# Optimization experiments

Measured on AMD Instinct MI355X. Metric: run time of the kernel, lower is better.

Reference implementation:

```python
import jax, jax.numpy as jnp
import numpy as np

B, T, C, H = 2, 2048, 1024, 16
D = C // H  # 64 per-head dim


def setup_inputs() -> dict:
    key = jax.random.key(0)
    ks = jax.random.split(key, 9)
    s = 1.0 / np.sqrt(C)
    return {
        "query_src": jax.random.normal(ks[0], (B, T, C), jnp.float32),
        "key_src": jax.random.normal(ks[1], (B, T, C), jnp.float32),
        "value_src": jax.random.normal(ks[2], (B, T, C), jnp.float32),
        "Wq": jax.random.normal(ks[3], (C, C), jnp.float32) * s,
        "Wk": jax.random.normal(ks[4], (C, C), jnp.float32) * s,
        "Wv": jax.random.normal(ks[5], (C, C), jnp.float32) * s,
        "Wo": jax.random.normal(ks[6], (C, C), jnp.float32) * s,
        "bo": jax.random.normal(ks[7], (C,), jnp.float32) * s,
    }


def reference(query_src, key_src, value_src, Wq, Wk, Wv, Wo, bo):
    # Linear layers: y = x @ W.T (torch nn.Linear convention)
    q = jnp.einsum('btc,dc->btd', query_src, Wq).reshape(B, T, H, D).transpose(0, 2, 1, 3)
    k = jnp.einsum('btc,dc->btd', key_src, Wk).reshape(B, T, H, D).transpose(0, 2, 1, 3)
    v = jnp.einsum('btc,dc->btd', value_src, Wv).reshape(B, T, H, D).transpose(0, 2, 1, 3)
    # scores: [B, H, T, T]
    scores = jnp.einsum('bhqd,bhkd->bhqk', q, k)
    # FAITHFUL quirk: original divides by d**(-0.5) => multiplies by sqrt(D)
    scores = scores * jnp.sqrt(jnp.asarray(D, scores.dtype))
    # FAITHFUL quirk: softmax over dim=1 == the HEAD axis
    attn = jax.nn.softmax(scores, axis=1)
    # dropout is identity in eval mode
    out = jnp.einsum('bhqk,bhkd->bhqd', attn, v)  # [B,H,T,D]
    out = out.transpose(0, 2, 1, 3).reshape(B, T, C)
    return jnp.einsum('btc,dc->btd', out, Wo) + bo
```

## Files before the change

### kernel.cpp

```cpp
#include <hip/hip_runtime.h>
#include <cmath>

namespace {

constexpr int B_ = 2;
constexpr int T_ = 2048;
constexpr int C_ = 1024;
constexpr int H_ = 16;
constexpr int D_ = 64;

typedef _Float16 half8 __attribute__((ext_vector_type(8)));
typedef _Float16 half4 __attribute__((ext_vector_type(4)));
typedef float f32x4 __attribute__((ext_vector_type(4)));

__device__ inline f32x4 vmax4(f32x4 a, f32x4 b) {
  f32x4 r;
  r[0] = fmaxf(a[0], b[0]); r[1] = fmaxf(a[1], b[1]);
  r[2] = fmaxf(a[2], b[2]); r[3] = fmaxf(a[3], b[3]);
  return r;
}

__device__ __forceinline__ void gload16(const _Float16* g, _Float16* l) {
  __builtin_amdgcn_global_load_lds(
      (const __attribute__((address_space(1))) unsigned int*)g,
      (__attribute__((address_space(3))) unsigned int*)l, 16, 0, 0);
}

__device__ __forceinline__ void lds_barrier() {
  asm volatile("s_waitcnt lgkmcnt(0)" ::: "memory");
  __builtin_amdgcn_s_barrier();
}

__global__ __launch_bounds__(256)
void cast7(const float* __restrict__ xq, const float* __restrict__ xk,
           const float* __restrict__ xv, const float* __restrict__ wq,
           const float* __restrict__ wk, const float* __restrict__ wv,
           const float* __restrict__ wo,
           _Float16* __restrict__ dxq, _Float16* __restrict__ dxk,
           _Float16* __restrict__ dxv, _Float16* __restrict__ dwq,
           _Float16* __restrict__ dwk, _Float16* __restrict__ dwv,
           _Float16* __restrict__ dwo) {
  constexpr size_t NX = (size_t)4 << 20;
  constexpr size_t NW = (size_t)1 << 20;
  size_t g = ((size_t)blockIdx.x * 256 + threadIdx.x) * 8;
  const float* s; _Float16* d; size_t off;
  if      (g <     NX)          { s = xq; d = dxq; off = g; }
  else if (g < 2 * NX)          { s = xk; d = dxk; off = g - NX; }
  else if (g < 3 * NX)          { s = xv; d = dxv; off = g - 2 * NX; }
  else if (g < 3 * NX + NW)     { s = wq; d = dwq; off = g - 3 * NX; }
  else if (g < 3 * NX + 2 * NW) { s = wk; d = dwk; off = g - 3 * NX - NW; }
  else if (g < 3 * NX + 3 * NW) { s = wv; d = dwv; off = g - 3 * NX - 2 * NW; }
  else                          { s = wo; d = dwo; off = g - 3 * NX - 3 * NW; }
  const float4 a = *(const float4*)(s + off);
  const float4 b = *(const float4*)(s + off + 4);
  half8 h;
  h[0] = (_Float16)a.x; h[1] = (_Float16)a.y; h[2] = (_Float16)a.z; h[3] = (_Float16)a.w;
  h[4] = (_Float16)b.x; h[5] = (_Float16)b.y; h[6] = (_Float16)b.z; h[7] = (_Float16)b.w;
  *(half8*)(d + off) = h;
}

__global__ __launch_bounds__(256, 3)
void gemm_f16nt(const _Float16* __restrict__ A0, const _Float16* __restrict__ A1,
                const _Float16* __restrict__ A2,
                const _Float16* __restrict__ W0, const _Float16* __restrict__ W1,
                const _Float16* __restrict__ W2,
                _Float16* __restrict__ Y0, _Float16* __restrict__ Y1,
                _Float16* __restrict__ Y2,
                float* __restrict__ Yf, const float* __restrict__ bias,
                int K, int N, int mode, float qsc) {
  __shared__ _Float16 sA[128 * 32];
  __shared__ _Float16 sW[128 * 32];

  const int tid  = threadIdx.x;
  const int lane = tid & 63;
  const int w    = tid >> 6;
  const int l15  = lane & 15;
  const int quad = lane >> 4;
  const int z    = blockIdx.z;
  const _Float16* A = (z == 0) ? A0 : (z == 1) ? A1 : A2;
  const _Float16* W = (z == 0) ? W0 : (z == 1) ? W1 : W2;
  _Float16*       Y = (z == 0) ? Y0 : (z == 1) ? Y1 : Y2;

  const int m0 = blockIdx.y * 128;
  const int n0 = blockIdx.x * 128;

  const int Rb  = lane >> 2;
  const int pch = lane & 3;
  const int lch = pch ^ ((Rb >> 1) & 3);
  const int swr = (l15 >> 1) & 3;

  f32x4 acc[4][4];
#pragma unroll
  for (int mt = 0; mt < 4; ++mt)
#pragma unroll
    for (int nt = 0; nt < 4; ++nt)
      acc[mt][nt] = (f32x4){0.f, 0.f, 0.f, 0.f};

  const int wm = (w >> 1) * 64;
  const int wn = (w & 1) * 64;

  for (int k0 = 0; k0 < K; k0 += 32) {
    __syncthreads();
#pragma unroll
    for (int j = 0; j < 2; ++j) {
      const int seg = w * 32 + j * 16;
      gload16(A + (size_t)(m0 + seg + Rb) * K + k0 + lch * 8, &sA[seg * 32]);
      gload16(W + (size_t)(n0 + seg + Rb) * K + k0 + lch * 8, &sW[seg * 32]);
    }
    __syncthreads();

    half8 af[4], wf[4];
#pragma unroll
    for (int mt = 0; mt < 4; ++mt) {
      const int R = wm + mt * 16 + l15;
      af[mt] = *(const half8*)&sA[R * 32 + (quad ^ swr) * 8];
    }
#pragma unroll
    for (int nt = 0; nt < 4; ++nt) {
      const int R = wn + nt * 16 + l15;
      wf[nt] = *(const half8*)&sW[R * 32 + (quad ^ swr) * 8];
    }
#pragma unroll
    for (int mt = 0; mt < 4; ++mt)
#pragma unroll
      for (int nt = 0; nt < 4; ++nt)
        acc[mt][nt] = __builtin_amdgcn_mfma_f32_16x16x32_f16(wf[nt], af[mt], acc[mt][nt], 0, 0, 0);
  }

  const float ysc = (mode == 0 && z == 0) ? qsc : 1.f;
#pragma unroll
  for (int mt = 0; mt < 4; ++mt)
#pragma unroll
    for (int nt = 0; nt < 4; ++nt) {
      const int m = m0 + wm + mt * 16 + l15;
      const int n = n0 + wn + nt * 16 + quad * 4;
      if (mode == 2) {
        float4 v;
        v.x = acc[mt][nt][0] + bias[n + 0];
        v.y = acc[mt][nt][1] + bias[n + 1];
        v.z = acc[mt][nt][2] + bias[n + 2];
        v.w = acc[mt][nt][3] + bias[n + 3];
        *(float4*)(Yf + (size_t)m * N + n) = v;
      } else {
        half4 hv;
#pragma unroll
        for (int r = 0; r < 4; ++r) hv[r] = (_Float16)(acc[mt][nt][r] * ysc);
        *(half4*)(Y + (size_t)m * N + n) = hv;
      }
    }
}

__global__ __launch_bounds__(256)
void transpose_v(const _Float16* __restrict__ Vh, _Float16* __restrict__ Vt) {
  constexpr int PAD = 1028;
  __shared__ _Float16 tile[16][PAD];
  const int b  = blockIdx.x >> 7;
  const int kt = blockIdx.x & 127;
  const int tid = threadIdx.x;

#pragma unroll
  for (int j = 0; j < 8; ++j) {
    const int ch = tid + 256 * j;
    const int t  = ch >> 7;
    const int c8 = ch & 127;
    *(half8*)&tile[t][c8 * 8] =
        *(const half8*)(Vh + ((size_t)b * T_ + kt * 16 + t) * C_ + c8 * 8);
  }
  __syncthreads();

#pragma unroll
  for (int j = 0; j < 8; ++j) {
    const int cc = tid + 256 * j;
    const int h  = cc >> 7;
    const int d  = (cc >> 1) & 63;
    const int th = (cc & 1) * 8;
    const int c  = h * 64 + d;
    half4 va, vb4;
#pragma unroll
    for (int i = 0; i < 4; ++i) va[i]  = tile[th + i][c];
#pragma unroll
    for (int i = 0; i < 4; ++i) vb4[i] = tile[th + 4 + i][c];
    const size_t tb = (((size_t)b * H_ + h) * 128 + kt) * 1024;
    const int nb = ((d >> 5) & 1) * 512 + ((th >> 2) * 16 + (d & 15)) * 8 +
                   ((d >> 4) & 1) * 4;
    *(half4*)(Vt + tb + nb) = va;
    *(half4*)(Vt + tb + nb + 128) = vb4;
  }
}

__global__ __launch_bounds__(1024, 4)
void attn_mfma(const _Float16* __restrict__ Qhp, const _Float16* __restrict__ Khp,
               const _Float16* __restrict__ Vtp, _Float16* __restrict__ OP,
               int nsplit) {
  __shared__ _Float16 sK[16 * 1024];
  __shared__ _Float16 sV[2][16][1024];
  __shared__ f32x4 redm[4][4][64];
  __shared__ f32x4 reds[4][4][64];

  const int tid  = threadIdx.x;
  const int lane = tid & 63;
  const int w    = tid >> 6;
  const int qt   = w >> 2;
  const int wg   = w & 3;
  const int l15  = lane & 15;
  const int quad = lane >> 4;
  const int cell = quad * 16 + l15;

  const int nbq   = B_ * (T_ / 64);
  const int split = blockIdx.x / nbq;
  const int bq    = blockIdx.x % nbq;
  const int b  = bq >> 5;
  const int q0 = (bq & 31) << 6;

  const size_t qrow = ((size_t)b * T_ + q0 + qt * 16 + l15) * C_;
  half8 qh[4][2];
#pragma unroll
  for (int hl = 0; hl < 4; ++hl)
#pragma unroll
    for (int kk = 0; kk < 2; ++kk)
      qh[hl][kk] = *(const half8*)(Qhp + qrow + (wg * 4 + hl) * 64 + kk * 32 + quad * 8);

  f32x4 oacc[4][4];
#pragma unroll
  for (int hl = 0; hl < 4; ++hl)
#pragma unroll
    for (int mt = 0; mt < 4; ++mt)
      oacc[hl][mt] = (f32x4){0.f, 0.f, 0.f, 0.f};

  const int kpb  = T_ / nsplit;
  const int k_lo = split * kpb;
  const int jt   = kpb / 16;

  const int kx  = (lane * 8) ^ ((w & 7) << 3);
  const _Float16* vhead = Vtp + ((size_t)b * H_ + w) * (128 * 1024);

  auto STAGE = [&](int j) {
    const int k0 = k_lo + j * 16;
    const size_t kr = ((size_t)b * T_ + k0 + w) * C_;
    gload16(Khp + kr + kx,       &sK[w * 1024]);
    gload16(Khp + kr + 512 + kx, &sK[w * 1024 + 512]);
    const _Float16* vsrc = vhead + (size_t)(k0 >> 4) * 1024;
    gload16(vsrc + lane * 8,       &sV[j & 1][w][0]);
    gload16(vsrc + lane * 8 + 512, &sV[j & 1][w][512]);
  };

  const int rsw   = (l15 & 7) << 3;
  const int hbase = wg * 256;

  STAGE(0);
  for (int j = 0; j < jt; ++j) {
    const int p = j & 1;
    __syncthreads();

    half8 akh[4][2];
#pragma unroll
    for (int hl = 0; hl < 4; ++hl)
#pragma unroll
      for (int kk = 0; kk < 2; ++kk)
        akh[hl][kk] = *(const half8*)&sK[l15 * 1024 +
            ((hbase + hl * 64 + kk * 32 + quad * 8) ^ rsw)];

    f32x4 s[4];
#pragma unroll
    for (int hl = 0; hl < 4; ++hl) s[hl] = (f32x4){0.f, 0.f, 0.f, 0.f};
#pragma unroll
    for (int hl = 0; hl < 4; ++hl)
#pragma unroll
      for (int kk = 0; kk < 2; ++kk)
        s[hl] = __builtin_amdgcn_mfma_f32_16x16x32_f16(akh[hl][kk], qh[hl][kk], s[hl], 0, 0, 0);

    redm[wg][qt][cell] = vmax4(vmax4(s[0], s[1]), vmax4(s[2], s[3]));
    lds_barrier();

    if (j + 1 < jt) STAGE(j + 1);

    const f32x4 gmax = vmax4(vmax4(redm[0][qt][cell], redm[1][qt][cell]),
                             vmax4(redm[2][qt][cell], redm[3][qt][cell]));
    f32x4 ps = (f32x4){0.f, 0.f, 0.f, 0.f};
#pragma unroll
    for (int hl = 0; hl < 4; ++hl)
#pragma unroll
      for (int r = 0; r < 4; ++r) {
        const float ev = __expf(s[hl][r] - gmax[r]);
        s[hl][r] = ev;
        ps[r] += ev;
      }
    reds[wg][qt][cell] = ps;
    lds_barrier();

    const f32x4 gs = reds[0][qt][cell] + reds[1][qt][cell] +
                     reds[2][qt][cell] + reds[3][qt][cell];
    f32x4 inv;
#pragma unroll
    for (int r = 0; r < 4; ++r) inv[r] = __builtin_amdgcn_rcpf(gs[r]);

    half4 pf[4];
#pragma unroll
    for (int hl = 0; hl < 4; ++hl)
#pragma unroll
      for (int r = 0; r < 4; ++r)
        pf[hl][r] = (_Float16)(s[hl][r] * inv[r]);

#pragma unroll
    for (int hl = 0; hl < 4; ++hl) {
      const half8 a0 = *(const half8*)&sV[p][wg * 4 + hl][cell * 8];
      const half8 a1 = *(const half8*)&sV[p][wg * 4 + hl][cell * 8 + 512];
      const half4 v0 = __builtin_shufflevector(a0, a0, 0, 1, 2, 3);
      const half4 v1 = __builtin_shufflevector(a0, a0, 4, 5, 6, 7);
      const half4 v2 = __builtin_shufflevector(a1, a1, 0, 1, 2, 3);
      const half4 v3 = __builtin_shufflevector(a1, a1, 4, 5, 6, 7);
      oacc[hl][0] = __builtin_amdgcn_mfma_f32_16x16x16f16(v0, pf[hl], oacc[hl][0], 0, 0, 0);
      oacc[hl][1] = __builtin_amdgcn_mfma_f32_16x16x16f16(v1, pf[hl], oacc[hl][1], 0, 0, 0);
      oacc[hl][2] = __builtin_amdgcn_mfma_f32_16x16x16f16(v2, pf[hl], oacc[hl][2], 0, 0, 0);
      oacc[hl][3] = __builtin_amdgcn_mfma_f32_16x16x16f16(v3, pf[hl], oacc[hl][3], 0, 0, 0);
    }
  }

  _Float16* op = OP + (size_t)split * ((size_t)B_ * T_ * C_);
  const size_t orow = ((size_t)b * T_ + q0 + qt * 16 + l15) * C_;
#pragma unroll
  for (int hl = 0; hl < 4; ++hl)
#pragma unroll
    for (int mt = 0; mt < 4; ++mt) {
      half4 hv;
#pragma unroll
      for (int r = 0; r < 4; ++r) hv[r] = (_Float16)oacc[hl][mt][r];
      *(half4*)(op + orow + (wg * 4 + hl) * 64 + mt * 16 + quad * 4) = hv;
    }
}

__global__ __launch_bounds__(256)
void reduce_oh(const _Float16* __restrict__ OP, _Float16* __restrict__ AOh,
               int nsplit, size_t n) {
  const size_t i = ((size_t)blockIdx.x * 256 + threadIdx.x) * 8;
  float a[8] = {};
  for (int s = 0; s < nsplit; ++s) {
    const half8 v = *(const half8*)(OP + (size_t)s * n + i);
#pragma unroll
    for (int r = 0; r < 8; ++r) a[r] += (float)v[r];
  }
  half8 o;
#pragma unroll
  for (int r = 0; r < 8; ++r) o[r] = (_Float16)a[r];
  *(half8*)(AOh + i) = o;
}

}

extern "C" void kernel_launch(void* const* d_in, const int* in_sizes, int n_in,
                              void* d_out, int out_size, void* d_ws, size_t ws_size,
                              hipStream_t stream) {
  const float* xq = (const float*)d_in[0];
  const float* xk = (const float*)d_in[1];
  const float* xv = (const float*)d_in[2];
  const float* Wq = (const float*)d_in[3];
  const float* Wk = (const float*)d_in[4];
  const float* Wv = (const float*)d_in[5];
  const float* Wo = (const float*)d_in[6];
  const float* bo = (const float*)d_in[7];
  float* out = (float*)d_out;

  const size_t MB   = 1ull << 20;
  const size_t nBTC = (size_t)B_ * T_ * C_;

  char* wsb = (char*)d_ws;
  _Float16* Qh  = (_Float16*)(wsb + 0 * MB);
  _Float16* Kh  = (_Float16*)(wsb + 8 * MB);
  _Float16* Vt  = (_Float16*)(wsb + 16 * MB);
  _Float16* vh  = (_Float16*)(wsb + 24 * MB);
  _Float16* AOh = (_Float16*)(wsb + 24 * MB);
  _Float16* xqh = (_Float16*)(wsb + 32 * MB);
  _Float16* xkh = (_Float16*)(wsb + 40 * MB);
  _Float16* xvh = (_Float16*)(wsb + 48 * MB);
  _Float16* OP  = (_Float16*)(wsb + 32 * MB);
  _Float16* Wqh = (_Float16*)(wsb + 64 * MB);
  _Float16* Wkh = (_Float16*)(wsb + 66 * MB);
  _Float16* Wvh = (_Float16*)(wsb + 68 * MB);
  _Float16* Woh = (_Float16*)(wsb + 70 * MB);

  const int nsplit = 4;
  const int M = B_ * T_;
  dim3 blk(256);

  cast7<<<dim3(8192), blk, 0, stream>>>(xq, xk, xv, Wq, Wk, Wv, Wo,
                                        xqh, xkh, xvh, Wqh, Wkh, Wvh, Woh);

  gemm_f16nt<<<dim3(C_ / 128, M / 128, 3), blk, 0, stream>>>(
      xqh, xkh, xvh, Wqh, Wkh, Wvh, Qh, Kh, vh,
      nullptr, nullptr, C_, C_, 0, 8.f);

  transpose_v<<<dim3(B_ * 128), blk, 0, stream>>>(vh, Vt);

  attn_mfma<<<dim3(B_ * (T_ / 64) * nsplit), dim3(1024), 0, stream>>>(
      Qh, Kh, Vt, OP, nsplit);

  reduce_oh<<<dim3((unsigned)(nBTC / 2048)), blk, 0, stream>>>(OP, AOh, nsplit, nBTC);

  gemm_f16nt<<<dim3(C_ / 128, M / 128, 1), blk, 0, stream>>>(
      AOh, nullptr, nullptr, Woh, nullptr, nullptr, nullptr, nullptr, nullptr,
      out, bo, C_, C_, 2, 1.f);
}
```

Measured before the change: 370.9 us.

## Merge head-softmax max/sum reductions into one barrier and precompute LDS pointers

Each wave now computes its local max and its exp-sum against that local max, then publishes both together. After a single LDS barrier it combines the four partials with rescaling (an online-softmax style merge), which removes one of the two barriers per key tile. The loop is unrolled by two with fixed double-buffer parities, and LDS/global addresses are precomputed as pointers advanced incrementally. This adds extra exp calls per row and assumes jt is even.

```diff
diff --git a/kernel.cpp b/kernel.cpp
--- a/kernel.cpp
+++ b/kernel.cpp
@@ -194,8 +194,7 @@
                int nsplit) {
   __shared__ _Float16 sK[16 * 1024];
   __shared__ _Float16 sV[2][16][1024];
-  __shared__ f32x4 redm[4][4][64];
-  __shared__ f32x4 reds[4][4][64];
+  __shared__ f32x4 red[2][4][4][64];
 
   const int tid  = threadIdx.x;
   const int lane = tid & 63;
@@ -204,7 +203,6 @@
   const int wg   = w & 3;
   const int l15  = lane & 15;
   const int quad = lane >> 4;
-  const int cell = quad * 16 + l15;
 
   const int nbq   = B_ * (T_ / 64);
   const int split = blockIdx.x / nbq;
@@ -231,35 +229,35 @@
   const int k_lo = split * kpb;
   const int jt   = kpb / 16;
 
-  const int kx  = (lane * 8) ^ ((w & 7) << 3);
-  const _Float16* vhead = Vtp + ((size_t)b * H_ + w) * (128 * 1024);
-
-  auto STAGE = [&](int j) {
-    const int k0 = k_lo + j * 16;
-    const size_t kr = ((size_t)b * T_ + k0 + w) * C_;
-    gload16(Khp + kr + kx,       &sK[w * 1024]);
-    gload16(Khp + kr + 512 + kx, &sK[w * 1024 + 512]);
-    const _Float16* vsrc = vhead + (size_t)(k0 >> 4) * 1024;
-    gload16(vsrc + lane * 8,       &sV[j & 1][w][0]);
-    gload16(vsrc + lane * 8 + 512, &sV[j & 1][w][512]);
+  const int rswb = (l15 & 7) << 4;
+  const char* kB0 = (const char*)sK + (l15 * 2048 + ((quad * 16) ^ rswb) + wg * 512);
+  const char* kB1 = (const char*)sK + (l15 * 2048 + (((64 + quad * 16)) ^ rswb) + wg * 512);
+  const char* vB  = (const char*)sV + (wg * 8192 + lane * 16);
+
+  const int kxel = (lane * 8) ^ ((w & 7) << 3);
+  const _Float16* kg = Khp + ((size_t)b * T_ + k_lo + w) * C_ + kxel;
+  const _Float16* vg = Vtp + ((size_t)b * H_ + w) * (128 * 1024) +
+                       (size_t)(k_lo >> 4) * 1024 + lane * 8;
+  _Float16* dK  = &sK[w * 1024];
+  _Float16* dV0 = &sV[0][w][0];
+  _Float16* dV1 = &sV[1][w][0];
+
+  auto STAGE = [&](_Float16* dv) {
+    gload16(kg, dK);       gload16(kg + 512, dK + 512);
+    gload16(vg, dv);       gload16(vg + 512, dv + 512);
+    kg += 16 * C_;
+    vg += 1024;
   };
 
-  const int rsw   = (l15 & 7) << 3;
-  const int hbase = wg * 256;
-
-  STAGE(0);
-  for (int j = 0; j < jt; ++j) {
-    const int p = j & 1;
+  auto tile = [&](int j, int p, _Float16* dvnext) {
     __syncthreads();
 
     half8 akh[4][2];
 #pragma unroll
-    for (int hl = 0; hl < 4; ++hl)
-#pragma unroll
-      for (int kk = 0; kk < 2; ++kk)
-        akh[hl][kk] = *(const half8*)&sK[l15 * 1024 +
-            ((hbase + hl * 64 + kk * 32 + quad * 8) ^ rsw)];
-
+    for (int hl = 0; hl < 4; ++hl) {
+      akh[hl][0] = *(const half8*)(kB0 + hl * 128);
+      akh[hl][1] = *(const half8*)(kB1 + hl * 128);
+    }
     f32x4 s[4];
 #pragma unroll
     for (int hl = 0; hl < 4; ++hl) s[hl] = (f32x4){0.f, 0.f, 0.f, 0.f};
@@ -269,42 +267,46 @@
       for (int kk = 0; kk < 2; ++kk)
         s[hl] = __builtin_amdgcn_mfma_f32_16x16x32_f16(akh[hl][kk], qh[hl][kk], s[hl], 0, 0, 0);
 
-    redm[wg][qt][cell] = vmax4(vmax4(s[0], s[1]), vmax4(s[2], s[3]));
-    lds_barrier();
-
-    if (j + 1 < jt) STAGE(j + 1);
-
-    const f32x4 gmax = vmax4(vmax4(redm[0][qt][cell], redm[1][qt][cell]),
-                             vmax4(redm[2][qt][cell], redm[3][qt][cell]));
+    const f32x4 mw = vmax4(vmax4(s[0], s[1]), vmax4(s[2], s[3]));
+    red[0][wg][qt][lane] = mw;
     f32x4 ps = (f32x4){0.f, 0.f, 0.f, 0.f};
 #pragma unroll
     for (int hl = 0; hl < 4; ++hl)
 #pragma unroll
       for (int r = 0; r < 4; ++r) {
-        const float ev = __expf(s[hl][r] - gmax[r]);
+        const float ev = __expf(s[hl][r] - mw[r]);
         s[hl][r] = ev;
         ps[r] += ev;
       }
-    reds[wg][qt][cell] = ps;
+    red[1][wg][qt][lane] = ps;
     lds_barrier();
 
-    const f32x4 gs = reds[0][qt][cell] + reds[1][qt][cell] +
-                     reds[2][qt][cell] + reds[3][qt][cell];
-    f32x4 inv;
-#pragma unroll
-    for (int r = 0; r < 4; ++r) inv[r] = __builtin_amdgcn_rcpf(gs[r]);
+    if (j + 1 < jt) STAGE(dvnext);
+
+    const f32x4 m0 = red[0][0][qt][lane], m1 = red[0][1][qt][lane];
+    const f32x4 m2 = red[0][2][qt][lane], m3 = red[0][3][qt][lane];
+    const f32x4 p0 = red[1][0][qt][lane], p1 = red[1][1][qt][lane];
+    const f32x4 p2 = red[1][2][qt][lane], p3 = red[1][3][qt][lane];
+    const f32x4 gm = vmax4(vmax4(m0, m1), vmax4(m2, m3));
+    f32x4 f;
+#pragma unroll
+    for (int r = 0; r < 4; ++r) {
+      const float t = p0[r] * __expf(m0[r] - gm[r]) + p1[r] * __expf(m1[r] - gm[r]) +
+                      p2[r] * __expf(m2[r] - gm[r]) + p3[r] * __expf(m3[r] - gm[r]);
+      f[r] = __expf(mw[r] - gm[r]) * __builtin_amdgcn_rcpf(t);
+    }
 
     half4 pf[4];
 #pragma unroll
     for (int hl = 0; hl < 4; ++hl)
 #pragma unroll
       for (int r = 0; r < 4; ++r)
-        pf[hl][r] = (_Float16)(s[hl][r] * inv[r]);
+        pf[hl][r] = (_Float16)(s[hl][r] * f[r]);
 
 #pragma unroll
     for (int hl = 0; hl < 4; ++hl) {
-      const half8 a0 = *(const half8*)&sV[p][wg * 4 + hl][cell * 8];
-      const half8 a1 = *(const half8*)&sV[p][wg * 4 + hl][cell * 8 + 512];
+      const half8 a0 = *(const half8*)(vB + p * 32768 + hl * 2048);
+      const half8 a1 = *(const half8*)(vB + p * 32768 + hl * 2048 + 1024);
       const half4 v0 = __builtin_shufflevector(a0, a0, 0, 1, 2, 3);
       const half4 v1 = __builtin_shufflevector(a0, a0, 4, 5, 6, 7);
       const half4 v2 = __builtin_shufflevector(a1, a1, 0, 1, 2, 3);
@@ -314,6 +316,12 @@
       oacc[hl][2] = __builtin_amdgcn_mfma_f32_16x16x16f16(v2, pf[hl], oacc[hl][2], 0, 0, 0);
       oacc[hl][3] = __builtin_amdgcn_mfma_f32_16x16x16f16(v3, pf[hl], oacc[hl][3], 0, 0, 0);
     }
+  };
+
+  STAGE(dV0);
+  for (int j = 0; j < jt; j += 2) {
+    tile(j,     0, dV1);
+    tile(j + 1, 1, dV0);
   }
 
   _Float16* op = OP + (size_t)split * ((size_t)B_ * T_ * C_);
```

New measurement: 426.9 us. +15.1%, slower.
